# Kernel optimization log

Hardware: AMD Instinct MI355X
Metric: run time of the kernel (lower is better)

Reference implementation:

```python
import jax, jax.numpy as jnp
import numpy as np

B, S, D_MODEL, N_HEAD, D_HEAD = 4, 2048, 512, 8, 64


def setup_inputs() -> dict:
    key = jax.random.key(0)
    ks = jax.random.split(key, 12)
    s = 0.02
    Q = jax.random.normal(ks[0], (B, S, D_MODEL), jnp.float32)
    K = jax.random.normal(ks[1], (B, S, D_MODEL), jnp.float32)
    V = jax.random.normal(ks[2], (B, S, D_MODEL), jnp.float32)
    # causal 0/1 mask, 1 = masked-out (scores get -1e9*mask)
    causal = jnp.triu(jnp.ones((S, S), jnp.float32), k=1)
    attn_mask = jnp.broadcast_to(causal, (B, S, S))
    Wq = jax.random.normal(ks[3], (D_MODEL, N_HEAD * D_HEAD), jnp.float32) * s
    bq = jnp.zeros((N_HEAD * D_HEAD,), jnp.float32)
    Wk = jax.random.normal(ks[4], (D_MODEL, N_HEAD * D_HEAD), jnp.float32) * s
    bk = jnp.zeros((N_HEAD * D_HEAD,), jnp.float32)
    Wv = jax.random.normal(ks[5], (D_MODEL, N_HEAD * D_HEAD), jnp.float32) * s
    bv = jnp.zeros((N_HEAD * D_HEAD,), jnp.float32)
    Wo = jax.random.normal(ks[6], (N_HEAD * D_HEAD, D_MODEL), jnp.float32) * s
    bo = jnp.zeros((D_MODEL,), jnp.float32)
    return {"Q": Q, "K": K, "V": V, "attn_mask": attn_mask,
            "Wq": Wq, "bq": bq, "Wk": Wk, "bk": bk,
            "Wv": Wv, "bv": bv, "Wo": Wo, "bo": bo}


def reference(Q, K, V, attn_mask, Wq, bq, Wk, bk, Wv, bv, Wo, bo):
    # project and split heads: [B,S,D] -> [B,H,S,Dh]
    def heads(x, W, b):
        return (x @ W + b).reshape(B, S, N_HEAD, D_HEAD).transpose(0, 2, 1, 3)

    Qh, Kh, Vh = heads(Q, Wq, bq), heads(K, Wk, bk), heads(V, Wv, bv)
    scale = jnp.sqrt(jnp.asarray(D_HEAD, jnp.float32))
    scores = jnp.einsum('bhqd,bhkd->bhqk', Qh, Kh) / scale  # [B,H,S,S]
    scores = scores - 1e9 * attn_mask[:, None, :, :]
    probs = jax.nn.softmax(scores, axis=-1)
    out = jnp.einsum('bhqk,bhkd->bhqd', probs, Vh)
    out = out.transpose(0, 2, 1, 3).reshape(B, S, N_HEAD * D_HEAD)
    return out @ Wo + bo
```

## Files before the change

### kernel.cpp

```cpp
#include <hip/hip_runtime.h>
#include <hip/hip_bf16.h>
#include <cstdint>
#include <cstddef>

#define B_DIM   4
#define S_DIM   2048
#define DMODEL  512
#define N_HEAD  8
#define D_HEAD  64
#define M_TOT   (B_DIM*S_DIM)

typedef __attribute__((ext_vector_type(8))) short bf16x8;
typedef __attribute__((ext_vector_type(4))) float f32x4;
typedef __attribute__((ext_vector_type(4))) unsigned short us4;

static __device__ __forceinline__ unsigned short f2bf(float x) {
  unsigned int u = __float_as_uint(x);
  unsigned int r = (u + 0x7fffu + ((u >> 16) & 1u)) >> 16;
  return (unsigned short)r;
}

static __device__ __forceinline__ void gl2lds16(const unsigned short* g, unsigned short* l) {
  __builtin_amdgcn_global_load_lds(
      (const __attribute__((address_space(1))) void*)g,
      (__attribute__((address_space(3))) void*)l, 16, 0, 0);
}

__global__ __launch_bounds__(256) void prep_kernel(
    const float* __restrict__ q, const float* __restrict__ k, const float* __restrict__ v,
    const float* __restrict__ wq, const float* __restrict__ wk,
    const float* __restrict__ wv, const float* __restrict__ wo,
    unsigned short* __restrict__ oq, unsigned short* __restrict__ ok,
    unsigned short* __restrict__ ov, unsigned short* __restrict__ wout)
{
  __shared__ float T[64][65];
  const int z = blockIdx.z;
  const int tid = threadIdx.x;
  if (z < 3) {
    const float* in  = (z==0)? q : (z==1)? k : v;
    unsigned short* out = (z==0)? oq : (z==1)? ok : ov;
    size_t i = ((size_t)blockIdx.x*256 + tid)*8;
    float4 a = *(const float4*)(in + i);
    float4 b = *(const float4*)(in + i + 4);
    us4 p0, p1;
    p0[0]=f2bf(a.x); p0[1]=f2bf(a.y); p0[2]=f2bf(a.z); p0[3]=f2bf(a.w);
    p1[0]=f2bf(b.x); p1[1]=f2bf(b.y); p1[2]=f2bf(b.z); p1[3]=f2bf(b.w);
    *(us4*)(out+i)   = p0;
    *(us4*)(out+i+4) = p1;
  } else {
    if (blockIdx.x >= 256) return;
    const int w = blockIdx.x >> 6, tile = blockIdx.x & 63;
    const float* W = (w==0)? wq : (w==1)? wk : (w==2)? wv : wo;
    unsigned short* O = wout + (size_t)w*DMODEL*DMODEL;
    const int k0 = (tile>>3)*64, n0 = (tile&7)*64;
    #pragma unroll
    for (int i=0;i<16;i++){
      int flat = tid + i*256; int r = flat>>6, c = flat&63;
      T[r][c] = W[(size_t)(k0+r)*DMODEL + n0 + c];
    }
    __syncthreads();
    #pragma unroll
    for (int i=0;i<16;i++){
      int flat = tid + i*256; int r = flat>>6, c = flat&63;
      O[(size_t)(n0+r)*DMODEL + k0 + c] = f2bf(T[c][r]);
    }
  }
}

__global__ __launch_bounds__(256) void proj_kernel(
    const unsigned short* __restrict__ Qbf, const unsigned short* __restrict__ Kbf,
    const unsigned short* __restrict__ Vbf, const unsigned short* __restrict__ Wtr,
    const float* __restrict__ bq, const float* __restrict__ bk, const float* __restrict__ bv,
    unsigned short* __restrict__ Qh, unsigned short* __restrict__ Kh, unsigned short* __restrict__ Vht)
{
  __shared__ __align__(16) unsigned short At[2][128*32];
  __shared__ __align__(16) unsigned short Bt[2][128*32];
  const int mode = blockIdx.z;
  const unsigned short* A  = (mode==0)? Qbf : (mode==1)? Kbf : Vbf;
  const unsigned short* Wt = Wtr + (size_t)mode*DMODEL*DMODEL;
  const float* bias = (mode==0)? bq : (mode==1)? bk : bv;
  const int tid = threadIdx.x, wave = tid>>6, lane = tid&63;
  const int g = lane>>4, ln = lane&15;
  const int mB = blockIdx.y*128, nB = blockIdx.x*128;
  const int mw = (wave>>1)*64,  nw = (wave&1)*64;
  const int srow = lane>>2, scolE = (lane&3)*8;
  const int cA = 2*wave, cB = 2*wave+1;

  #define STG_G(buf, k0_)                                                      \
    do {                                                                       \
      gl2lds16(A  + (size_t)(mB + cA*16 + srow)*DMODEL + (k0_) + scolE, &At[buf][cA*512]); \
      gl2lds16(A  + (size_t)(mB + cB*16 + srow)*DMODEL + (k0_) + scolE, &At[buf][cB*512]); \
      gl2lds16(Wt + (size_t)(nB + cA*16 + srow)*DMODEL + (k0_) + scolE, &Bt[buf][cA*512]); \
      gl2lds16(Wt + (size_t)(nB + cB*16 + srow)*DMODEL + (k0_) + scolE, &Bt[buf][cB*512]); \
    } while (0)

  f32x4 acc[4][4];
  #pragma unroll
  for (int i=0;i<4;i++)
    #pragma unroll
    for (int jj=0;jj<4;jj++) acc[i][jj]=(f32x4){0.f,0.f,0.f,0.f};

  STG_G(0, 0);
  __syncthreads();
  for (int s=0; s<16; ++s){
    const int cur = s&1;
    if (s+1 < 16) STG_G(cur^1, (s+1)*32);
    bf16x8 a[4], bb[4];
    #pragma unroll
    for (int rf=0;rf<4;rf++) a[rf]  = *(const bf16x8*)(&At[cur][(mw + rf*16 + ln)*32 + g*8]);
    #pragma unroll
    for (int cf=0;cf<4;cf++) bb[cf] = *(const bf16x8*)(&Bt[cur][(nw + cf*16 + ln)*32 + g*8]);
    __builtin_amdgcn_s_setprio(1);
    #pragma unroll
    for (int rf=0;rf<4;rf++)
      #pragma unroll
      for (int cf=0;cf<4;cf++)
        acc[rf][cf] = __builtin_amdgcn_mfma_f32_16x16x32_bf16(a[rf], bb[cf], acc[rf][cf], 0,0,0);
    __builtin_amdgcn_s_setprio(0);
    __syncthreads();
  }
  #undef STG_G

  const int m0 = mB + mw, n0 = nB + nw;
  float bvv[4];
  #pragma unroll
  for (int cf=0;cf<4;cf++) bvv[cf] = bias[n0 + cf*16 + ln];
  const float QSC = 0.18033688011112042f;

  if (mode <= 1) {
    unsigned short* O = (mode==0)? Qh : Kh;
    const float sc = (mode==0)? QSC : 1.0f;
    #pragma unroll
    for (int rf=0;rf<4;rf++){
      int m = m0 + rf*16 + 4*g;
      int b2 = m >> 11, sdx = m & (S_DIM-1);
      #pragma unroll
      for (int cf=0;cf<4;cf++){
        int n = n0 + cf*16 + ln;
        int h = n >> 6, d = n & 63;
        size_t base = ((size_t)(b2*N_HEAD + h)*S_DIM + sdx)*D_HEAD + d;
        #pragma unroll
        for (int r=0;r<4;r++)
          O[base + (size_t)r*D_HEAD] = f2bf((acc[rf][cf][r] + bvv[cf]) * sc);
      }
    }
  } else {
    #pragma unroll
    for (int rf=0;rf<4;rf++){
      int m = m0 + rf*16 + 4*g;
      int b2 = m >> 11, sdx = m & (S_DIM-1);
      #pragma unroll
      for (int cf=0;cf<4;cf++){
        int n = n0 + cf*16 + ln;
        int h = n >> 6, d = n & 63;
        us4 pk;
        #pragma unroll
        for (int r=0;r<4;r++) pk[r] = f2bf(acc[rf][cf][r] + bvv[cf]);
        *(us4*)&Vht[((size_t)(b2*N_HEAD + h)*D_HEAD + d)*S_DIM + sdx] = pk;
      }
    }
  }
}

__global__ __launch_bounds__(256) void attn_kernel(
    const unsigned short* __restrict__ Qh, const unsigned short* __restrict__ Kh,
    const unsigned short* __restrict__ Vht, unsigned short* __restrict__ AO)
{
  __shared__ __align__(16) unsigned short Kt[2][64*64];
  __shared__ __align__(16) unsigned short Vt[2][64*64];
  __shared__ __align__(16) unsigned short Plds[4][16][72];

  const int tid = threadIdx.x, wave = tid>>6, lane = tid&63;
  const int g = lane>>4, ln = lane&15;
  const int j = blockIdx.x;
  const int xcd = j & 7, sblk = j >> 3;
  const int bh = xcd*4 + (sblk & 3);
  const int qt = 31 - (sblk >> 2);
  const int qrow0 = qt*64 + wave*16;
  const int q_i = qrow0 + ln;
  const int nit = qt + 1;
  const int b = bh >> 3, h = bh & 7;

  const unsigned short* Qp = Qh  + (size_t)bh*S_DIM*D_HEAD;
  const unsigned short* Kp = Kh  + (size_t)bh*S_DIM*D_HEAD;
  const unsigned short* Vp = Vht + (size_t)bh*D_HEAD*S_DIM;

  const int lrow = lane >> 3;
  const int scol = (((lane & 7) ^ lrow) << 3);
  const int swz  = (lane & 7) << 3;
  const int c0 = 2*wave, c1 = 2*wave + 1;

  #define STG_KV(buf, k0_)                                                     \
    do {                                                                       \
      gl2lds16(Kp + ((size_t)(k0_) + c0*8 + lrow)*64 + scol, &Kt[buf][c0*512]); \
      gl2lds16(Kp + ((size_t)(k0_) + c1*8 + lrow)*64 + scol, &Kt[buf][c1*512]); \
      gl2lds16(Vp + (size_t)(c0*8 + lrow)*S_DIM + (k0_) + scol, &Vt[buf][c0*512]); \
      gl2lds16(Vp + (size_t)(c1*8 + lrow)*S_DIM + (k0_) + scol, &Vt[buf][c1*512]); \
    } while (0)

  bf16x8 qf0 = *(const bf16x8*)(Qp + (size_t)(qrow0+ln)*D_HEAD + 8*g);
  bf16x8 qf1 = *(const bf16x8*)(Qp + (size_t)(qrow0+ln)*D_HEAD + 32 + 8*g);

  f32x4 o[4];
  #pragma unroll
  for (int cc=0;cc<4;cc++) o[cc] = (f32x4){0.f,0.f,0.f,0.f};
  float lsum = 0.f;

  STG_KV(0, 0);
  __syncthreads();

  for (int it = 0; it < nit; ++it) {
    const int cur = it & 1;
    if (it + 1 < nit) STG_KV(cur^1, (it+1)*64);
    const unsigned short* Kc = Kt[cur];
    const unsigned short* Vc = Vt[cur];

    f32x4 s[4];
    __builtin_amdgcn_s_setprio(1);
    #pragma unroll
    for (int i=0;i<4;i++){
      const int r = i*16 + ln;
      bf16x8 ka0 = *(const bf16x8*)(Kc + r*64 + ((g*8) ^ swz));
      bf16x8 ka1 = *(const bf16x8*)(Kc + r*64 + ((32 + g*8) ^ swz));
      f32x4 z = (f32x4){0.f,0.f,0.f,0.f};
      z = __builtin_amdgcn_mfma_f32_16x16x32_bf16(ka0, qf0, z, 0,0,0);
      z = __builtin_amdgcn_mfma_f32_16x16x32_bf16(ka1, qf1, z, 0,0,0);
      s[i] = z;
    }
    __builtin_amdgcn_s_setprio(0);
    if (it == nit-1) {
      const int k0 = it*64;
      #pragma unroll
      for (int i=0;i<4;i++)
        #pragma unroll
        for (int r=0;r<4;r++)
          if (k0 + i*16 + 4*g + r > q_i) s[i][r] = -1e30f;
    }
    float p[4][4];
    #pragma unroll
    for (int i=0;i<4;i++)
      #pragma unroll
      for (int r=0;r<4;r++){
        float e = __builtin_amdgcn_exp2f(s[i][r]);
        p[i][r] = e; lsum += e;
      }
    #pragma unroll
    for (int i=0;i<4;i++){
      us4 pk;
      pk[0]=f2bf(p[i][0]); pk[1]=f2bf(p[i][1]); pk[2]=f2bf(p[i][2]); pk[3]=f2bf(p[i][3]);
      *(us4*)&Plds[wave][ln][i*16 + 4*g] = pk;
    }
    bf16x8 pa0 = *(const bf16x8*)&Plds[wave][ln][8*g];
    bf16x8 pa1 = *(const bf16x8*)&Plds[wave][ln][32 + 8*g];
    __builtin_amdgcn_s_setprio(1);
    #pragma unroll
    for (int cc=0;cc<4;cc++){
      const int r = cc*16 + ln;
      bf16x8 vb0 = *(const bf16x8*)(Vc + r*64 + ((g*8) ^ swz));
      bf16x8 vb1 = *(const bf16x8*)(Vc + r*64 + ((32 + g*8) ^ swz));
      o[cc] = __builtin_amdgcn_mfma_f32_16x16x32_bf16(pa0, vb0, o[cc], 0,0,0);
      o[cc] = __builtin_amdgcn_mfma_f32_16x16x32_bf16(pa1, vb1, o[cc], 0,0,0);
    }
    __builtin_amdgcn_s_setprio(0);
    __syncthreads();
  }
  #undef STG_KV

  float lt = lsum;
  lt += __shfl_xor(lt, 16, 64);
  lt += __shfl_xor(lt, 32, 64);
  #pragma unroll
  for (int r=0;r<4;r++){
    float lq  = __shfl(lt, 4*g + r, 64);
    float inv = 1.0f / lq;
    int srow2 = qrow0 + 4*g + r;
    size_t base = ((size_t)b*S_DIM + srow2)*DMODEL + h*D_HEAD;
    #pragma unroll
    for (int cc=0;cc<4;cc++)
      AO[base + cc*16 + ln] = f2bf(o[cc][r]*inv);
  }
}

__global__ __launch_bounds__(256) void outproj_kernel(
    const unsigned short* __restrict__ AO, const unsigned short* __restrict__ Wt,
    const float* __restrict__ bo, float* __restrict__ Out)
{
  __shared__ __align__(16) unsigned short At[2][128*32];
  __shared__ __align__(16) unsigned short Bt[2][128*32];
  const int tid = threadIdx.x, wave = tid>>6, lane = tid&63;
  const int g = lane>>4, ln = lane&15;
  const int mB = blockIdx.y*128, nB = blockIdx.x*128;
  const int mw = (wave>>1)*64,  nw = (wave&1)*64;
  const int srow = lane>>2, scolE = (lane&3)*8;
  const int cA = 2*wave, cB = 2*wave+1;

  #define STG_G(buf, k0_)                                                      \
    do {                                                                       \
      gl2lds16(AO + (size_t)(mB + cA*16 + srow)*DMODEL + (k0_) + scolE, &At[buf][cA*512]); \
      gl2lds16(AO + (size_t)(mB + cB*16 + srow)*DMODEL + (k0_) + scolE, &At[buf][cB*512]); \
      gl2lds16(Wt + (size_t)(nB + cA*16 + srow)*DMODEL + (k0_) + scolE, &Bt[buf][cA*512]); \
      gl2lds16(Wt + (size_t)(nB + cB*16 + srow)*DMODEL + (k0_) + scolE, &Bt[buf][cB*512]); \
    } while (0)

  f32x4 acc[4][4];
  #pragma unroll
  for (int i=0;i<4;i++)
    #pragma unroll
    for (int jj=0;jj<4;jj++) acc[i][jj]=(f32x4){0.f,0.f,0.f,0.f};

  STG_G(0, 0);
  __syncthreads();
  for (int s=0; s<16; ++s){
    const int cur = s&1;
    if (s+1 < 16) STG_G(cur^1, (s+1)*32);
    bf16x8 a[4], bb[4];
    #pragma unroll
    for (int rf=0;rf<4;rf++) a[rf]  = *(const bf16x8*)(&At[cur][(mw + rf*16 + ln)*32 + g*8]);
    #pragma unroll
    for (int cf=0;cf<4;cf++) bb[cf] = *(const bf16x8*)(&Bt[cur][(nw + cf*16 + ln)*32 + g*8]);
    __builtin_amdgcn_s_setprio(1);
    #pragma unroll
    for (int rf=0;rf<4;rf++)
      #pragma unroll
      for (int cf=0;cf<4;cf++)
        acc[rf][cf] = __builtin_amdgcn_mfma_f32_16x16x32_bf16(a[rf], bb[cf], acc[rf][cf], 0,0,0);
    __builtin_amdgcn_s_setprio(0);
    __syncthreads();
  }
  #undef STG_G

  const int m0 = mB + mw, n0 = nB + nw;
  float bvv[4];
  #pragma unroll
  for (int cf=0;cf<4;cf++) bvv[cf] = bo[n0 + cf*16 + ln];
  #pragma unroll
  for (int rf=0;rf<4;rf++){
    #pragma unroll
    for (int cf=0;cf<4;cf++){
      int n = n0 + cf*16 + ln;
      #pragma unroll
      for (int r=0;r<4;r++){
        int m = m0 + rf*16 + 4*g + r;
        Out[(size_t)m*DMODEL + n] = acc[rf][cf][r] + bvv[cf];
      }
    }
  }
}

extern "C" void kernel_launch(void* const* d_in, const int* in_sizes, int n_in,
                              void* d_out, int out_size, void* d_ws, size_t ws_size,
                              hipStream_t stream)
{
  const float* Q  = (const float*)d_in[0];
  const float* K  = (const float*)d_in[1];
  const float* V  = (const float*)d_in[2];
  const float* Wq = (const float*)d_in[4];
  const float* bq = (const float*)d_in[5];
  const float* Wk = (const float*)d_in[6];
  const float* bk = (const float*)d_in[7];
  const float* Wv = (const float*)d_in[8];
  const float* bv = (const float*)d_in[9];
  const float* Wo = (const float*)d_in[10];
  const float* bo = (const float*)d_in[11];

  unsigned short* ws = (unsigned short*)d_ws;
  const size_t TEN = (size_t)M_TOT * DMODEL;
  unsigned short* Qbf = ws;
  unsigned short* Kbf = Qbf + TEN;
  unsigned short* Vbf = Kbf + TEN;
  unsigned short* Wtr = Vbf + TEN;
  unsigned short* Qh  = Wtr + (size_t)4*DMODEL*DMODEL;
  unsigned short* Kh  = Qh + TEN;
  unsigned short* Vht = Kh + TEN;
  unsigned short* AO  = Vht + TEN;

  prep_kernel   <<<dim3(2048,1,4), 256, 0, stream>>>(Q,K,V,Wq,Wk,Wv,Wo,Qbf,Kbf,Vbf,Wtr);
  proj_kernel   <<<dim3(4,64,3),   256, 0, stream>>>(Qbf,Kbf,Vbf,Wtr,bq,bk,bv,Qh,Kh,Vht);
  attn_kernel   <<<dim3(1024),     256, 0, stream>>>(Qh,Kh,Vht,AO);
  outproj_kernel<<<dim3(4,64),     256, 0, stream>>>(AO, Wtr + (size_t)3*DMODEL*DMODEL, bo, (float*)d_out);
}
```

Measured before the change: 221.1 us.

## Fuse fp32-to-bf16 input conversion into projection GEMM and widen attention blocks

Drops the separate activation conversion pass. The projection kernel now loads fp32 Q/K/V tiles directly into LDS with an XOR swizzle and converts them to bf16 in registers using v_cvt_pk_bf16_f32. This removes a full write and read of three bf16 activation tensors. The attention kernel moves to 512-thread blocks covering 128 query rows, so each staged K/V tile is shared by twice as many waves, and causal masking now applies per wave. Packed conversion also replaces the manual rounding for P, at the cost of doubled fp32 LDS footprint and more conversion work in the GEMM inner loop.

```diff
diff --git a/kernel.cpp b/kernel.cpp
--- a/kernel.cpp
+++ b/kernel.cpp
@@ -13,6 +13,8 @@
 typedef __attribute__((ext_vector_type(8))) short bf16x8;
 typedef __attribute__((ext_vector_type(4))) float f32x4;
 typedef __attribute__((ext_vector_type(4))) unsigned short us4;
+typedef __attribute__((ext_vector_type(2))) unsigned int u32x2;
+typedef __attribute__((ext_vector_type(4))) unsigned int u32x4;
 
 static __device__ __forceinline__ unsigned short f2bf(float x) {
   unsigned int u = __float_as_uint(x);
@@ -20,76 +22,73 @@
   return (unsigned short)r;
 }
 
+static __device__ __forceinline__ unsigned int cvtpk(float lo, float hi) {
+  unsigned int r;
+  asm("v_cvt_pk_bf16_f32 %0, %1, %2" : "=v"(r) : "v"(lo), "v"(hi));
+  return r;
+}
+
 static __device__ __forceinline__ void gl2lds16(const unsigned short* g, unsigned short* l) {
   __builtin_amdgcn_global_load_lds(
       (const __attribute__((address_space(1))) void*)g,
       (__attribute__((address_space(3))) void*)l, 16, 0, 0);
 }
-
-__global__ __launch_bounds__(256) void prep_kernel(
-    const float* __restrict__ q, const float* __restrict__ k, const float* __restrict__ v,
+static __device__ __forceinline__ void gl2lds16f(const float* g, float* l) {
+  __builtin_amdgcn_global_load_lds(
+      (const __attribute__((address_space(1))) void*)g,
+      (__attribute__((address_space(3))) void*)l, 16, 0, 0);
+}
+
+__global__ __launch_bounds__(256) void wprep_kernel(
     const float* __restrict__ wq, const float* __restrict__ wk,
     const float* __restrict__ wv, const float* __restrict__ wo,
-    unsigned short* __restrict__ oq, unsigned short* __restrict__ ok,
-    unsigned short* __restrict__ ov, unsigned short* __restrict__ wout)
+    unsigned short* __restrict__ out)
 {
   __shared__ float T[64][65];
-  const int z = blockIdx.z;
+  const int w = blockIdx.x >> 6, tile = blockIdx.x & 63;
+  const float* W = (w==0)? wq : (w==1)? wk : (w==2)? wv : wo;
+  unsigned short* O = out + (size_t)w*DMODEL*DMODEL;
+  const int k0 = (tile>>3)*64, n0 = (tile&7)*64;
   const int tid = threadIdx.x;
-  if (z < 3) {
-    const float* in  = (z==0)? q : (z==1)? k : v;
-    unsigned short* out = (z==0)? oq : (z==1)? ok : ov;
-    size_t i = ((size_t)blockIdx.x*256 + tid)*8;
-    float4 a = *(const float4*)(in + i);
-    float4 b = *(const float4*)(in + i + 4);
-    us4 p0, p1;
-    p0[0]=f2bf(a.x); p0[1]=f2bf(a.y); p0[2]=f2bf(a.z); p0[3]=f2bf(a.w);
-    p1[0]=f2bf(b.x); p1[1]=f2bf(b.y); p1[2]=f2bf(b.z); p1[3]=f2bf(b.w);
-    *(us4*)(out+i)   = p0;
-    *(us4*)(out+i+4) = p1;
-  } else {
-    if (blockIdx.x >= 256) return;
-    const int w = blockIdx.x >> 6, tile = blockIdx.x & 63;
-    const float* W = (w==0)? wq : (w==1)? wk : (w==2)? wv : wo;
-    unsigned short* O = wout + (size_t)w*DMODEL*DMODEL;
-    const int k0 = (tile>>3)*64, n0 = (tile&7)*64;
-    #pragma unroll
-    for (int i=0;i<16;i++){
-      int flat = tid + i*256; int r = flat>>6, c = flat&63;
-      T[r][c] = W[(size_t)(k0+r)*DMODEL + n0 + c];
-    }
-    __syncthreads();
-    #pragma unroll
-    for (int i=0;i<16;i++){
-      int flat = tid + i*256; int r = flat>>6, c = flat&63;
-      O[(size_t)(n0+r)*DMODEL + k0 + c] = f2bf(T[c][r]);
-    }
+  #pragma unroll
+  for (int i=0;i<16;i++){
+    int flat = tid + i*256; int r = flat>>6, c = flat&63;
+    T[r][c] = W[(size_t)(k0+r)*DMODEL + n0 + c];
+  }
+  __syncthreads();
+  #pragma unroll
+  for (int i=0;i<16;i++){
+    int flat = tid + i*256; int r = flat>>6, c = flat&63;
+    O[(size_t)(n0+r)*DMODEL + k0 + c] = f2bf(T[c][r]);
   }
 }
 
 __global__ __launch_bounds__(256) void proj_kernel(
-    const unsigned short* __restrict__ Qbf, const unsigned short* __restrict__ Kbf,
-    const unsigned short* __restrict__ Vbf, const unsigned short* __restrict__ Wtr,
+    const float* __restrict__ Qf, const float* __restrict__ Kf,
+    const float* __restrict__ Vf, const unsigned short* __restrict__ Wtr,
     const float* __restrict__ bq, const float* __restrict__ bk, const float* __restrict__ bv,
     unsigned short* __restrict__ Qh, unsigned short* __restrict__ Kh, unsigned short* __restrict__ Vht)
 {
-  __shared__ __align__(16) unsigned short At[2][128*32];
+  __shared__ __align__(16) float          Af[2][128*32];
   __shared__ __align__(16) unsigned short Bt[2][128*32];
   const int mode = blockIdx.z;
-  const unsigned short* A  = (mode==0)? Qbf : (mode==1)? Kbf : Vbf;
+  const float* A = (mode==0)? Qf : (mode==1)? Kf : Vf;
   const unsigned short* Wt = Wtr + (size_t)mode*DMODEL*DMODEL;
   const float* bias = (mode==0)? bq : (mode==1)? bk : bv;
   const int tid = threadIdx.x, wave = tid>>6, lane = tid&63;
   const int g = lane>>4, ln = lane&15;
   const int mB = blockIdx.y*128, nB = blockIdx.x*128;
   const int mw = (wave>>1)*64,  nw = (wave&1)*64;
+  const int lrowA = lane>>3, suF = ((lane&7) ^ (lane>>3))*4;
   const int srow = lane>>2, scolE = (lane&3)*8;
   const int cA = 2*wave, cB = 2*wave+1;
 
-  #define STG_G(buf, k0_)                                                      \
+  #define STG(buf, k0_)                                                        \
     do {                                                                       \
-      gl2lds16(A  + (size_t)(mB + cA*16 + srow)*DMODEL + (k0_) + scolE, &At[buf][cA*512]); \
-      gl2lds16(A  + (size_t)(mB + cB*16 + srow)*DMODEL + (k0_) + scolE, &At[buf][cB*512]); \
+      _Pragma("unroll")                                                        \
+      for (int q=0;q<4;q++)                                                    \
+        gl2lds16f(A + (size_t)(mB + (wave*4+q)*8 + lrowA)*DMODEL + (k0_) + suF,\
+                  &Af[buf][(wave*4+q)*256]);                                   \
       gl2lds16(Wt + (size_t)(nB + cA*16 + srow)*DMODEL + (k0_) + scolE, &Bt[buf][cA*512]); \
       gl2lds16(Wt + (size_t)(nB + cB*16 + srow)*DMODEL + (k0_) + scolE, &Bt[buf][cB*512]); \
     } while (0)
@@ -100,14 +99,26 @@
     #pragma unroll
     for (int jj=0;jj<4;jj++) acc[i][jj]=(f32x4){0.f,0.f,0.f,0.f};
 
-  STG_G(0, 0);
+  STG(0, 0);
   __syncthreads();
   for (int s=0; s<16; ++s){
     const int cur = s&1;
-    if (s+1 < 16) STG_G(cur^1, (s+1)*32);
+    if (s+1 < 16) STG(cur^1, (s+1)*32);
     bf16x8 a[4], bb[4];
     #pragma unroll
-    for (int rf=0;rf<4;rf++) a[rf]  = *(const bf16x8*)(&At[cur][(mw + rf*16 + ln)*32 + g*8]);
+    for (int rf=0;rf<4;rf++){
+      const int row = mw + rf*16 + ln;
+      const int u0 = (2*g)   ^ (ln&7);
+      const int u1 = (2*g+1) ^ (ln&7);
+      f32x4 x0 = *(const f32x4*)&Af[cur][row*32 + u0*4];
+      f32x4 x1 = *(const f32x4*)&Af[cur][row*32 + u1*4];
+      union { u32x4 u; bf16x8 b; } t;
+      t.u[0] = cvtpk(x0[0], x0[1]);
+      t.u[1] = cvtpk(x0[2], x0[3]);
+      t.u[2] = cvtpk(x1[0], x1[1]);
+      t.u[3] = cvtpk(x1[2], x1[3]);
+      a[rf] = t.b;
+    }
     #pragma unroll
     for (int cf=0;cf<4;cf++) bb[cf] = *(const bf16x8*)(&Bt[cur][(nw + cf*16 + ln)*32 + g*8]);
     __builtin_amdgcn_s_setprio(1);
@@ -119,7 +130,7 @@
     __builtin_amdgcn_s_setprio(0);
     __syncthreads();
   }
-  #undef STG_G
+  #undef STG
 
   const int m0 = mB + mw, n0 = nB + nw;
   float bvv[4];
@@ -162,23 +173,23 @@
   }
 }
 
-__global__ __launch_bounds__(256) void attn_kernel(
+__global__ __launch_bounds__(512,4) void attn_kernel(
     const unsigned short* __restrict__ Qh, const unsigned short* __restrict__ Kh,
     const unsigned short* __restrict__ Vht, unsigned short* __restrict__ AO)
 {
   __shared__ __align__(16) unsigned short Kt[2][64*64];
   __shared__ __align__(16) unsigned short Vt[2][64*64];
-  __shared__ __align__(16) unsigned short Plds[4][16][72];
+  __shared__ __align__(16) unsigned short Plds[8][16][72];
 
   const int tid = threadIdx.x, wave = tid>>6, lane = tid&63;
   const int g = lane>>4, ln = lane&15;
   const int j = blockIdx.x;
-  const int xcd = j & 7, sblk = j >> 3;
-  const int bh = xcd*4 + (sblk & 3);
-  const int qt = 31 - (sblk >> 2);
-  const int qrow0 = qt*64 + wave*16;
+  const int xcd = j & 7, rest = j >> 3;
+  const int bh = xcd*4 + (rest & 3);
+  const int t  = 15 - (rest >> 2);
+  const int qrow0 = t*128 + wave*16;
   const int q_i = qrow0 + ln;
-  const int nit = qt + 1;
+  const int nit = 2*t + 2;
   const int b = bh >> 3, h = bh & 7;
 
   const unsigned short* Qp = Qh  + (size_t)bh*S_DIM*D_HEAD;
@@ -188,14 +199,13 @@
   const int lrow = lane >> 3;
   const int scol = (((lane & 7) ^ lrow) << 3);
   const int swz  = (lane & 7) << 3;
-  const int c0 = 2*wave, c1 = 2*wave + 1;
-
-  #define STG_KV(buf, k0_)                                                     \
-    do {                                                                       \
-      gl2lds16(Kp + ((size_t)(k0_) + c0*8 + lrow)*64 + scol, &Kt[buf][c0*512]); \
-      gl2lds16(Kp + ((size_t)(k0_) + c1*8 + lrow)*64 + scol, &Kt[buf][c1*512]); \
-      gl2lds16(Vp + (size_t)(c0*8 + lrow)*S_DIM + (k0_) + scol, &Vt[buf][c0*512]); \
-      gl2lds16(Vp + (size_t)(c1*8 + lrow)*S_DIM + (k0_) + scol, &Vt[buf][c1*512]); \
+  const unsigned short* kg = Kp + (size_t)(wave*8 + lrow)*64 + scol;
+  const unsigned short* vg = Vp + (size_t)(wave*8 + lrow)*S_DIM + scol;
+
+  #define STG_KV(buf, k0_)                                   \
+    do {                                                     \
+      gl2lds16(kg + (size_t)(k0_)*64, &Kt[buf][wave*512]);   \
+      gl2lds16(vg + (k0_),            &Vt[buf][wave*512]);   \
     } while (0)
 
   bf16x8 qf0 = *(const bf16x8*)(Qp + (size_t)(qrow0+ln)*D_HEAD + 8*g);
@@ -228,8 +238,8 @@
       s[i] = z;
     }
     __builtin_amdgcn_s_setprio(0);
-    if (it == nit-1) {
-      const int k0 = it*64;
+    const int k0 = it*64;
+    if (k0 + 63 > q_i - ln) {
       #pragma unroll
       for (int i=0;i<4;i++)
         #pragma unroll
@@ -246,9 +256,10 @@
       }
     #pragma unroll
     for (int i=0;i<4;i++){
-      us4 pk;
-      pk[0]=f2bf(p[i][0]); pk[1]=f2bf(p[i][1]); pk[2]=f2bf(p[i][2]); pk[3]=f2bf(p[i][3]);
-      *(us4*)&Plds[wave][ln][i*16 + 4*g] = pk;
+      u32x2 pk2;
+      pk2[0] = cvtpk(p[i][0], p[i][1]);
+      pk2[1] = cvtpk(p[i][2], p[i][3]);
+      *(u32x2*)&Plds[wave][ln][i*16 + 4*g] = pk2;
     }
     bf16x8 pa0 = *(const bf16x8*)&Plds[wave][ln][8*g];
     bf16x8 pa1 = *(const bf16x8*)&Plds[wave][ln][32 + 8*g];
@@ -365,17 +376,14 @@
 
   unsigned short* ws = (unsigned short*)d_ws;
   const size_t TEN = (size_t)M_TOT * DMODEL;
-  unsigned short* Qbf = ws;
-  unsigned short* Kbf = Qbf + TEN;
-  unsigned short* Vbf = Kbf + TEN;
-  unsigned short* Wtr = Vbf + TEN;
+  unsigned short* Wtr = ws;
   unsigned short* Qh  = Wtr + (size_t)4*DMODEL*DMODEL;
   unsigned short* Kh  = Qh + TEN;
   unsigned short* Vht = Kh + TEN;
   unsigned short* AO  = Vht + TEN;
 
-  prep_kernel   <<<dim3(2048,1,4), 256, 0, stream>>>(Q,K,V,Wq,Wk,Wv,Wo,Qbf,Kbf,Vbf,Wtr);
-  proj_kernel   <<<dim3(4,64,3),   256, 0, stream>>>(Qbf,Kbf,Vbf,Wtr,bq,bk,bv,Qh,Kh,Vht);
-  attn_kernel   <<<dim3(1024),     256, 0, stream>>>(Qh,Kh,Vht,AO);
-  outproj_kernel<<<dim3(4,64),     256, 0, stream>>>(AO, Wtr + (size_t)3*DMODEL*DMODEL, bo, (float*)d_out);
-}
+  wprep_kernel  <<<dim3(256),    256, 0, stream>>>(Wq,Wk,Wv,Wo,Wtr);
+  proj_kernel   <<<dim3(4,64,3), 256, 0, stream>>>(Q,K,V,Wtr,bq,bk,bv,Qh,Kh,Vht);
+  attn_kernel   <<<dim3(512),    512, 0, stream>>>(Qh,Kh,Vht,AO);
+  outproj_kernel<<<dim3(4,64),   256, 0, stream>>>(AO, Wtr + (size_t)3*DMODEL*DMODEL, bo, (float*)d_out);
+}
```

Result: slower. 226.9 us (+2.6%).
